# Performance work log

Hardware: AMD Instinct MI355X
Metric: run time of the kernel (lower is better)

## Reference

```python
import jax, jax.numpy as jnp
import numpy as np

D, N_T, N, N_H = 8, 2048, 64, 8
STD_E = 0.02
STD_Q = 0.02


def setup_inputs() -> dict:
    key = jax.random.key(0)
    k1, k2, k3 = jax.random.split(key, 3)
    r_prime = jax.random.normal(k1, (D, N_T, N), dtype=jnp.float32)
    Q = jax.random.normal(k2, (N_H, N, N), dtype=jnp.float32) * STD_Q
    E = jax.random.normal(k3, (N_H, N, N), dtype=jnp.float32) * STD_E
    return {"r_prime": r_prime, "Q": Q, "E": E}


def reference(r_prime, Q, E):
    # r_prime: (b=d, t=n_t, i=n); Q, E: (h, i, j)
    n_t = r_prime.shape[1]
    # Omega[b,h,t,u] = sum_ij r'[b,t,i] Q[h,i,j] r'[b,u,j]
    Qr = jnp.einsum('hij,buj->bhui', Q, r_prime)          # (b, h, u, i)
    Omega = jnp.einsum('bti,bhui->bhtu', r_prime, Qr)     # (b, h, t, u)
    # causal lower-triangular mask (t >= u)
    mask = jnp.tril(jnp.ones((n_t, n_t), dtype=r_prime.dtype))
    Omega = Omega * mask  # broadcast over (b, h)
    # r[b,t,i] = sum_{h,u,j} Omega[b,h,t,u] E[h,i,j] r'[b,u,j]
    Er = jnp.einsum('hij,buj->bhui', E, r_prime)          # (b, h, u, i)
    r = jnp.einsum('bhtu,bhui->bti', Omega, Er)           # (b, t, i)
    return r
```

## Files before the change

### kernel.cpp

```cpp
#include <hip/hip_runtime.h>

#define D_B 8
#define N_T 2048
#define NN  64
#define N_H 8
#define N_C 32
#define NP  72

typedef __bf16 bf16;
typedef bf16 bf16x8 __attribute__((ext_vector_type(8)));
typedef bf16 bf16x4 __attribute__((ext_vector_type(4)));
typedef float f32x4 __attribute__((ext_vector_type(4)));

static __device__ __forceinline__ f32x4 mfma16(bf16x8 a, bf16x8 b, f32x4 c) {
    return __builtin_amdgcn_mfma_f32_16x16x32_bf16(a, b, c, 0, 0, 0);
}

static __device__ __forceinline__ bf16x8 ldcvt8(const float* p) {
    const f32x4 v0 = *(const f32x4*)p;
    const f32x4 v1 = *(const f32x4*)(p + 4);
    bf16x8 r;
#pragma unroll
    for (int k = 0; k < 4; k++) { r[k] = (bf16)v0[k]; r[4 + k] = (bf16)v1[k]; }
    return r;
}

__global__ __launch_bounds__(256, 4) void k_dg(
    const float* __restrict__ rp, const float* __restrict__ Qm,
    const float* __restrict__ Em,
    bf16* __restrict__ dGq, bf16* __restrict__ Rbf,
    bf16* __restrict__ Qrd, bf16* __restrict__ Erd)
{
    __shared__ bf16 Ql[64 * NP];
    __shared__ bf16 El[64 * NP];
    __shared__ bf16 QT[64 * NP];
    __shared__ bf16 ET[64 * NP];
    const int b = blockIdx.x, c = blockIdx.y, qt = blockIdx.z;
    const int tid = threadIdx.x;
    const int w = tid >> 6, l = tid & 63, q = l >> 4, l16 = l & 15;
    const int row = tid >> 2, col = (tid & 3) * 16;

    const float* rrow = rp + ((size_t)b * N_T + c * 64 + w * 16 + l16) * NN;
    const bf16x8 a0 = ldcvt8(rrow + q * 8);
    const bf16x8 a1 = ldcvt8(rrow + 32 + q * 8);

    if (qt == 0) {
        const float* src = rp + ((size_t)b * N_T + c * 64 + row) * NN + col;
        bf16* d = Rbf + ((size_t)b * N_T + c * 64 + row) * NN + col;
        *(bf16x8*)d       = ldcvt8(src);
        *(bf16x8*)(d + 8) = ldcvt8(src + 8);
    }

    f32x4 dacc[4];
#pragma unroll
    for (int ns = 0; ns < 4; ns++) { f32x4 z = {0.f, 0.f, 0.f, 0.f}; dacc[ns] = z; }

    for (int hh = 0; hh < 2; hh++) {
        const int h = qt * 2 + hh;
        {
            const float* qs = Qm + (size_t)h * 4096 + row * 64 + col;
            const float* es = Em + (size_t)h * 4096 + row * 64 + col;
            *(bf16x8*)&Ql[row * NP + col]     = ldcvt8(qs);
            *(bf16x8*)&Ql[row * NP + col + 8] = ldcvt8(qs + 8);
            *(bf16x8*)&El[row * NP + col]     = ldcvt8(es);
            *(bf16x8*)&El[row * NP + col + 8] = ldcvt8(es + 8);
        }
        __syncthreads();
        const size_t tb = (((size_t)(b * N_C + c)) * N_H + h) * 4096;
#pragma unroll
        for (int ns = 0; ns < 4; ns++) {
            bf16x8 b0 = *(const bf16x8*)&Ql[(ns * 16 + l16) * NP + q * 8];
            bf16x8 b1 = *(const bf16x8*)&Ql[(ns * 16 + l16) * NP + 32 + q * 8];
            f32x4 z = {0.f, 0.f, 0.f, 0.f};
            f32x4 s = mfma16(a0, b0, z);
            s = mfma16(a1, b1, s);
            bf16x4 p;
#pragma unroll
            for (int r = 0; r < 4; r++) p[r] = (bf16)s[r];
#pragma unroll
            for (int r = 0; r < 4; r++)
                Qrd[tb + (w * 16 + q * 4 + r) * 64 + ns * 16 + l16] = p[r];
            *(bf16x4*)&QT[(ns * 16 + l16) * NP + w * 16 + q * 4] = p;
            b0 = *(const bf16x8*)&El[(ns * 16 + l16) * NP + q * 8];
            b1 = *(const bf16x8*)&El[(ns * 16 + l16) * NP + 32 + q * 8];
            f32x4 s2 = mfma16(a0, b0, z);
            s2 = mfma16(a1, b1, s2);
#pragma unroll
            for (int r = 0; r < 4; r++) p[r] = (bf16)s2[r];
            *(bf16x4*)&ET[(ns * 16 + l16) * NP + w * 16 + q * 4] = p;
        }
        __syncthreads();
        {
            const bf16x8 qa0 = *(const bf16x8*)&QT[(w * 16 + l16) * NP + q * 8];
            const bf16x8 qa1 = *(const bf16x8*)&QT[(w * 16 + l16) * NP + 32 + q * 8];
#pragma unroll
            for (int ns = 0; ns < 4; ns++) {
                const bf16x8 e0 = *(const bf16x8*)&ET[(ns * 16 + l16) * NP + q * 8];
                const bf16x8 e1 = *(const bf16x8*)&ET[(ns * 16 + l16) * NP + 32 + q * 8];
                dacc[ns] = mfma16(qa0, e0, dacc[ns]);
                dacc[ns] = mfma16(qa1, e1, dacc[ns]);
            }
        }
        {
            const bf16x8 v0 = *(const bf16x8*)&ET[row * NP + col];
            const bf16x8 v1 = *(const bf16x8*)&ET[row * NP + col + 8];
            bf16* d = Erd + tb + row * 64 + col;
            *(bf16x8*)d = v0;
            *(bf16x8*)(d + 8) = v1;
        }
        __syncthreads();
    }
#pragma unroll
    for (int ns = 0; ns < 4; ns++) {
        bf16x4 p;
#pragma unroll
        for (int r = 0; r < 4; r++) p[r] = (bf16)dacc[ns][r];
        *(bf16x4*)&QT[(ns * 16 + l16) * NP + w * 16 + q * 4] = p;
    }
    __syncthreads();
    {
        bf16* dst = dGq + (((size_t)(b * N_C + c)) * 4 + qt) * 4096 + row * 64 + col;
        *(bf16x8*)dst       = *(const bf16x8*)&QT[row * NP + col];
        *(bf16x8*)(dst + 8) = *(const bf16x8*)&QT[row * NP + col + 8];
    }
}

__global__ __launch_bounds__(256, 4) void k_fold(const bf16* __restrict__ dGq,
                                                 bf16* __restrict__ dG8)
{
    const int b = blockIdx.x, c = blockIdx.y;
    const size_t base = ((size_t)(b * N_C + c)) * 4 * 4096 + threadIdx.x * 16;
    float s[16];
#pragma unroll
    for (int k = 0; k < 16; k++) s[k] = 0.f;
#pragma unroll
    for (int qt = 0; qt < 4; qt++) {
        const bf16x8 v0 = *(const bf16x8*)(dGq + base + (size_t)qt * 4096);
        const bf16x8 v1 = *(const bf16x8*)(dGq + base + (size_t)qt * 4096 + 8);
#pragma unroll
        for (int k = 0; k < 8; k++) { s[k] += (float)v0[k]; s[8 + k] += (float)v1[k]; }
    }
    bf16x8 o0, o1;
#pragma unroll
    for (int k = 0; k < 8; k++) { o0[k] = (bf16)s[k]; o1[k] = (bf16)s[8 + k]; }
    bf16* dst = dG8 + (size_t)(b * N_C + c) * 4096 + threadIdx.x * 16;
    *(bf16x8*)dst = o0;
    *(bf16x8*)(dst + 8) = o1;
}

template <int NU>
static __device__ __forceinline__ void head_iter(
    const bf16* __restrict__ Qh, const bf16* __restrict__ Eh,
    bf16* __restrict__ Sw, const bf16x8 ra0, const bf16x8 ra1,
    int l16, int q, int tbase, f32x4 (&acc)[4])
{
#pragma unroll
    for (int nu = 0; nu < NU; nu++) {
        const bf16x8 b0 = *(const bf16x8*)&Qh[(nu * 16 + l16) * 64 + q * 8];
        const bf16x8 b1 = *(const bf16x8*)&Qh[(nu * 16 + l16) * 64 + 32 + q * 8];
        f32x4 z = {0.f, 0.f, 0.f, 0.f};
        f32x4 sv = mfma16(ra0, b0, z);
        sv = mfma16(ra1, b1, sv);
        const int u_loc = nu * 16 + l16;
#pragma unroll
        for (int r = 0; r < 4; r++) {
            const int t_loc = tbase + q * 4 + r;
            Sw[(q * 4 + r) * NP + u_loc] = (u_loc <= t_loc) ? (bf16)sv[r] : (bf16)0.f;
        }
    }
    const bf16x8 sa0 = *(const bf16x8*)&Sw[l16 * NP + q * 8];
#pragma unroll
    for (int ns = 0; ns < 4; ns++) {
        const bf16x8 e0 = *(const bf16x8*)&Eh[(ns * 16 + l16) * 64 + q * 8];
        acc[ns] = mfma16(sa0, e0, acc[ns]);
    }
    if (NU == 4) {
        const bf16x8 sa1 = *(const bf16x8*)&Sw[l16 * NP + 32 + q * 8];
#pragma unroll
        for (int ns = 0; ns < 4; ns++) {
            const bf16x8 e1 = *(const bf16x8*)&Eh[(ns * 16 + l16) * 64 + 32 + q * 8];
            acc[ns] = mfma16(sa1, e1, acc[ns]);
        }
    }
}

__global__ __launch_bounds__(256, 4) void k_out(
    const bf16* __restrict__ dG8, const bf16* __restrict__ Rbf,
    const bf16* __restrict__ Qrd, const bf16* __restrict__ Erd,
    float* __restrict__ out)
{
    __shared__ bf16 Gb[64 * NP];
    __shared__ bf16 Sl[4 * 2 * 16 * NP];
    __shared__ float Ob[32 * 65];
    const int b = blockIdx.x, c = blockIdx.y, half = blockIdx.z;
    const int tid = threadIdx.x;
    const int w = tid >> 6, l = tid & 63, q = l >> 4, l16 = l & 15;
    const int s = w & 1, g = w >> 1;

    const int trow = c * 64 + half * 32 + s * 16 + l16;
    const bf16x8 ra0 = *(const bf16x8*)&Rbf[((size_t)b * N_T + trow) * NN + q * 8];
    const bf16x8 ra1 = *(const bf16x8*)&Rbf[((size_t)b * N_T + trow) * NN + 32 + q * 8];

    float run[16];
#pragma unroll
    for (int k = 0; k < 16; k++) run[k] = 0.f;
    {
        const bf16* base = dG8 + (size_t)b * N_C * 4096 + tid * 16;
        int t = 0;
        for (; t + 4 <= c; t += 4) {
            bf16x8 v[4][2];
#pragma unroll
            for (int j = 0; j < 4; j++) {
                v[j][0] = *(const bf16x8*)(base + (size_t)(t + j) * 4096);
                v[j][1] = *(const bf16x8*)(base + (size_t)(t + j) * 4096 + 8);
            }
#pragma unroll
            for (int j = 0; j < 4; j++)
#pragma unroll
                for (int k = 0; k < 8; k++) {
                    run[k] += (float)v[j][0][k];
                    run[8 + k] += (float)v[j][1][k];
                }
        }
        for (; t < c; t++) {
            const bf16x8 v0 = *(const bf16x8*)(base + (size_t)t * 4096);
            const bf16x8 v1 = *(const bf16x8*)(base + (size_t)t * 4096 + 8);
#pragma unroll
            for (int k = 0; k < 8; k++) { run[k] += (float)v0[k]; run[8 + k] += (float)v1[k]; }
        }
    }

    bf16* Sw0 = Sl + (w * 2 + 0) * 16 * NP;
    bf16* Sw1 = Sl + (w * 2 + 1) * 16 * NP;
    const int tbase = half * 32 + s * 16;
    const size_t hb = (((size_t)(b * N_C + c)) * N_H + g * 4) * 4096;
    const bf16* Qg = Qrd + hb;
    const bf16* Eg = Erd + hb;
    f32x4 acc[4];
#pragma unroll
    for (int ns = 0; ns < 4; ns++) { f32x4 z = {0.f, 0.f, 0.f, 0.f}; acc[ns] = z; }

    if (half) {
#pragma unroll
        for (int hh = 0; hh < 4; hh++)
            head_iter<4>(Qg + (size_t)hh * 4096, Eg + (size_t)hh * 4096,
                         (hh & 1) ? Sw1 : Sw0, ra0, ra1, l16, q, tbase, acc);
    } else {
#pragma unroll
        for (int hh = 0; hh < 4; hh++)
            head_iter<2>(Qg + (size_t)hh * 4096, Eg + (size_t)hh * 4096,
                         (hh & 1) ? Sw1 : Sw0, ra0, ra1, l16, q, tbase, acc);
    }

    {
        bf16x8 o0, o1;
#pragma unroll
        for (int k = 0; k < 8; k++) { o0[k] = (bf16)run[k]; o1[k] = (bf16)run[8 + k]; }
        *(bf16x8*)&Gb[(tid >> 2) * NP + (tid & 3) * 16] = o0;
        *(bf16x8*)&Gb[(tid >> 2) * NP + (tid & 3) * 16 + 8] = o1;
    }
    if (g == 0) {
#pragma unroll
        for (int ns = 0; ns < 4; ns++)
#pragma unroll
            for (int r = 0; r < 4; r++)
                Ob[(s * 16 + q * 4 + r) * 65 + ns * 16 + l16] = acc[ns][r];
    }
    __syncthreads();
    if (g == 1) {
#pragma unroll
        for (int ns = 0; ns < 4; ns++) {
            const bf16x8 g0 = *(const bf16x8*)&Gb[(ns * 16 + l16) * NP + q * 8];
            const bf16x8 g1 = *(const bf16x8*)&Gb[(ns * 16 + l16) * NP + 32 + q * 8];
            acc[ns] = mfma16(ra0, g0, acc[ns]);
            acc[ns] = mfma16(ra1, g1, acc[ns]);
        }
        const int t0 = c * 64 + half * 32;
#pragma unroll
        for (int ns = 0; ns < 4; ns++)
#pragma unroll
            for (int r = 0; r < 4; r++) {
                const float sum = acc[ns][r] + Ob[(s * 16 + q * 4 + r) * 65 + ns * 16 + l16];
                out[((size_t)b * N_T + t0 + s * 16 + q * 4 + r) * NN + ns * 16 + l16] = sum;
            }
    }
}

extern "C" void kernel_launch(void* const* d_in, const int* in_sizes, int n_in,
                              void* d_out, int out_size, void* d_ws, size_t ws_size,
                              hipStream_t stream) {
    const float* rp = (const float*)d_in[0];
    const float* Qm = (const float*)d_in[1];
    const float* Em = (const float*)d_in[2];
    float* out = (float*)d_out;

    bf16* dGq = (bf16*)d_ws;
    bf16* Rbf = dGq + (size_t)D_B * N_C * 4 * 4096;
    bf16* Qrd = Rbf + (size_t)D_B * N_T * NN;
    bf16* Erd = Qrd + (size_t)D_B * N_C * N_H * 4096;
    bf16* dG8 = Erd + (size_t)D_B * N_C * N_H * 4096;

    k_dg<<<dim3(D_B, N_C, 4), 256, 0, stream>>>(rp, Qm, Em, dGq, Rbf, Qrd, Erd);
    k_fold<<<dim3(D_B, N_C), 256, 0, stream>>>(dGq, dG8);
    k_out<<<dim3(D_B, N_C, 2), 256, 0, stream>>>(dG8, Rbf, Qrd, Erd, out);
}
```

Baseline: 102.9 us.

## Fold head-quarter partials via fp32 atomics and move prefix scan to its own kernel

k_dg now accumulates its four per-quarter partial dG tiles directly into an fp32 buffer with atomicAdd, which removes the bf16 partial buffer and the separate fold pass; a memset is added to zero that buffer first. The causal prefix sum over earlier chunks, which every k_out block used to redo, moves into a new k_scan kernel that writes one bf16 prefix tile per chunk. k_out then reads its prefix tile straight from global memory instead of scanning and staging it in LDS. The cost is many scalar fp32 atomics, doubled read bandwidth in the scan from fp32 storage, and an extra memset on the stream.

```diff
diff --git a/kernel.cpp b/kernel.cpp
--- a/kernel.cpp
+++ b/kernel.cpp
@@ -28,7 +28,7 @@
 __global__ __launch_bounds__(256, 4) void k_dg(
     const float* __restrict__ rp, const float* __restrict__ Qm,
     const float* __restrict__ Em,
-    bf16* __restrict__ dGq, bf16* __restrict__ Rbf,
+    float* __restrict__ dG8, bf16* __restrict__ Rbf,
     bf16* __restrict__ Qrd, bf16* __restrict__ Erd)
 {
     __shared__ bf16 Ql[64 * NP];
@@ -119,31 +119,49 @@
     }
     __syncthreads();
     {
-        bf16* dst = dGq + (((size_t)(b * N_C + c)) * 4 + qt) * 4096 + row * 64 + col;
-        *(bf16x8*)dst       = *(const bf16x8*)&QT[row * NP + col];
-        *(bf16x8*)(dst + 8) = *(const bf16x8*)&QT[row * NP + col + 8];
-    }
-}
-
-__global__ __launch_bounds__(256, 4) void k_fold(const bf16* __restrict__ dGq,
-                                                 bf16* __restrict__ dG8)
+        float* dst = dG8 + ((size_t)(b * N_C + c)) * 4096 + row * 64 + col;
+#pragma unroll
+        for (int k = 0; k < 16; k++)
+            atomicAdd(dst + k, (float)QT[row * NP + col + k]);
+    }
+}
+
+__global__ __launch_bounds__(256, 4) void k_scan(const float* __restrict__ dG8,
+                                                 bf16* __restrict__ Gc)
 {
     const int b = blockIdx.x, c = blockIdx.y;
-    const size_t base = ((size_t)(b * N_C + c)) * 4 * 4096 + threadIdx.x * 16;
-    float s[16];
-#pragma unroll
-    for (int k = 0; k < 16; k++) s[k] = 0.f;
-#pragma unroll
-    for (int qt = 0; qt < 4; qt++) {
-        const bf16x8 v0 = *(const bf16x8*)(dGq + base + (size_t)qt * 4096);
-        const bf16x8 v1 = *(const bf16x8*)(dGq + base + (size_t)qt * 4096 + 8);
-#pragma unroll
-        for (int k = 0; k < 8; k++) { s[k] += (float)v0[k]; s[8 + k] += (float)v1[k]; }
+    const int tid = threadIdx.x;
+    float run[16];
+#pragma unroll
+    for (int k = 0; k < 16; k++) run[k] = 0.f;
+    const float* base = dG8 + (size_t)b * N_C * 4096 + tid * 16;
+    int t = 0;
+    for (; t + 4 <= c; t += 4) {
+        f32x4 v[4][4];
+#pragma unroll
+        for (int j = 0; j < 4; j++)
+#pragma unroll
+            for (int m = 0; m < 4; m++)
+                v[j][m] = *(const f32x4*)(base + (size_t)(t + j) * 4096 + m * 4);
+#pragma unroll
+        for (int j = 0; j < 4; j++)
+#pragma unroll
+            for (int m = 0; m < 4; m++)
+#pragma unroll
+                for (int k = 0; k < 4; k++) run[m * 4 + k] += v[j][m][k];
+    }
+    for (; t < c; t++) {
+#pragma unroll
+        for (int m = 0; m < 4; m++) {
+            const f32x4 v = *(const f32x4*)(base + (size_t)t * 4096 + m * 4);
+#pragma unroll
+            for (int k = 0; k < 4; k++) run[m * 4 + k] += v[k];
+        }
     }
     bf16x8 o0, o1;
 #pragma unroll
-    for (int k = 0; k < 8; k++) { o0[k] = (bf16)s[k]; o1[k] = (bf16)s[8 + k]; }
-    bf16* dst = dG8 + (size_t)(b * N_C + c) * 4096 + threadIdx.x * 16;
+    for (int k = 0; k < 8; k++) { o0[k] = (bf16)run[k]; o1[k] = (bf16)run[8 + k]; }
+    bf16* dst = Gc + (size_t)(b * N_C + c) * 4096 + tid * 16;
     *(bf16x8*)dst = o0;
     *(bf16x8*)(dst + 8) = o1;
 }
@@ -185,11 +203,10 @@
 }
 
 __global__ __launch_bounds__(256, 4) void k_out(
-    const bf16* __restrict__ dG8, const bf16* __restrict__ Rbf,
+    const bf16* __restrict__ Gc, const bf16* __restrict__ Rbf,
     const bf16* __restrict__ Qrd, const bf16* __restrict__ Erd,
     float* __restrict__ out)
 {
-    __shared__ bf16 Gb[64 * NP];
     __shared__ bf16 Sl[4 * 2 * 16 * NP];
     __shared__ float Ob[32 * 65];
     const int b = blockIdx.x, c = blockIdx.y, half = blockIdx.z;
@@ -200,35 +217,6 @@
     const int trow = c * 64 + half * 32 + s * 16 + l16;
     const bf16x8 ra0 = *(const bf16x8*)&Rbf[((size_t)b * N_T + trow) * NN + q * 8];
     const bf16x8 ra1 = *(const bf16x8*)&Rbf[((size_t)b * N_T + trow) * NN + 32 + q * 8];
-
-    float run[16];
-#pragma unroll
-    for (int k = 0; k < 16; k++) run[k] = 0.f;
-    {
-        const bf16* base = dG8 + (size_t)b * N_C * 4096 + tid * 16;
-        int t = 0;
-        for (; t + 4 <= c; t += 4) {
-            bf16x8 v[4][2];
-#pragma unroll
-            for (int j = 0; j < 4; j++) {
-                v[j][0] = *(const bf16x8*)(base + (size_t)(t + j) * 4096);
-                v[j][1] = *(const bf16x8*)(base + (size_t)(t + j) * 4096 + 8);
-            }
-#pragma unroll
-            for (int j = 0; j < 4; j++)
-#pragma unroll
-                for (int k = 0; k < 8; k++) {
-                    run[k] += (float)v[j][0][k];
-                    run[8 + k] += (float)v[j][1][k];
-                }
-        }
-        for (; t < c; t++) {
-            const bf16x8 v0 = *(const bf16x8*)(base + (size_t)t * 4096);
-            const bf16x8 v1 = *(const bf16x8*)(base + (size_t)t * 4096 + 8);
-#pragma unroll
-            for (int k = 0; k < 8; k++) { run[k] += (float)v0[k]; run[8 + k] += (float)v1[k]; }
-        }
-    }
 
     bf16* Sw0 = Sl + (w * 2 + 0) * 16 * NP;
     bf16* Sw1 = Sl + (w * 2 + 1) * 16 * NP;
@@ -252,12 +240,15 @@
                          (hh & 1) ? Sw1 : Sw0, ra0, ra1, l16, q, tbase, acc);
     }
 
-    {
-        bf16x8 o0, o1;
-#pragma unroll
-        for (int k = 0; k < 8; k++) { o0[k] = (bf16)run[k]; o1[k] = (bf16)run[8 + k]; }
-        *(bf16x8*)&Gb[(tid >> 2) * NP + (tid & 3) * 16] = o0;
-        *(bf16x8*)&Gb[(tid >> 2) * NP + (tid & 3) * 16 + 8] = o1;
+    if (g == 1) {
+        const bf16* Gt = Gc + (size_t)(b * N_C + c) * 4096;
+#pragma unroll
+        for (int ns = 0; ns < 4; ns++) {
+            const bf16x8 g0 = *(const bf16x8*)&Gt[(ns * 16 + l16) * 64 + q * 8];
+            const bf16x8 g1 = *(const bf16x8*)&Gt[(ns * 16 + l16) * 64 + 32 + q * 8];
+            acc[ns] = mfma16(ra0, g0, acc[ns]);
+            acc[ns] = mfma16(ra1, g1, acc[ns]);
+        }
     }
     if (g == 0) {
 #pragma unroll
@@ -268,13 +259,6 @@
     }
     __syncthreads();
     if (g == 1) {
-#pragma unroll
-        for (int ns = 0; ns < 4; ns++) {
-            const bf16x8 g0 = *(const bf16x8*)&Gb[(ns * 16 + l16) * NP + q * 8];
-            const bf16x8 g1 = *(const bf16x8*)&Gb[(ns * 16 + l16) * NP + 32 + q * 8];
-            acc[ns] = mfma16(ra0, g0, acc[ns]);
-            acc[ns] = mfma16(ra1, g1, acc[ns]);
-        }
         const int t0 = c * 64 + half * 32;
 #pragma unroll
         for (int ns = 0; ns < 4; ns++)
@@ -294,13 +278,14 @@
     const float* Em = (const float*)d_in[2];
     float* out = (float*)d_out;
 
-    bf16* dGq = (bf16*)d_ws;
-    bf16* Rbf = dGq + (size_t)D_B * N_C * 4 * 4096;
+    float* dG8 = (float*)d_ws;
+    bf16* Gc  = (bf16*)(dG8 + (size_t)D_B * N_C * 4096);
+    bf16* Rbf = Gc + (size_t)D_B * N_C * 4096;
     bf16* Qrd = Rbf + (size_t)D_B * N_T * NN;
     bf16* Erd = Qrd + (size_t)D_B * N_C * N_H * 4096;
-    bf16* dG8 = Erd + (size_t)D_B * N_C * N_H * 4096;
-
-    k_dg<<<dim3(D_B, N_C, 4), 256, 0, stream>>>(rp, Qm, Em, dGq, Rbf, Qrd, Erd);
-    k_fold<<<dim3(D_B, N_C), 256, 0, stream>>>(dGq, dG8);
-    k_out<<<dim3(D_B, N_C, 2), 256, 0, stream>>>(dG8, Rbf, Qrd, Erd, out);
-}
+
+    hipMemsetAsync(dG8, 0, (size_t)D_B * N_C * 4096 * sizeof(float), stream);
+    k_dg<<<dim3(D_B, N_C, 4), 256, 0, stream>>>(rp, Qm, Em, dG8, Rbf, Qrd, Erd);
+    k_scan<<<dim3(D_B, N_C), 256, 0, stream>>>(dG8, Gc);
+    k_out<<<dim3(D_B, N_C, 2), 256, 0, stream>>>(Gc, Rbf, Qrd, Erd, out);
+}
```

New measurement: 301.2 us. 193% more time.
